# Kernel optimization log

Hardware: AMD Instinct MI355X
Metric: run time of the kernel (lower is better)

The kernel has to match this reference:

```python
import jax, jax.numpy as jnp
import numpy as np

B, T, D_MODEL, WINDOW = 2, 2048, 512, 32


def setup_inputs() -> dict:
    key = jax.random.key(0)
    ks = jax.random.split(key, 5)
    s = 1.0 / np.sqrt(D_MODEL)
    x = jax.random.normal(ks[0], (B, T, D_MODEL), jnp.float32)
    # torch.nn.Linear convention: weight [out_features, in_features], y = x @ W.T + b
    w_qkv = jax.random.uniform(ks[1], (3 * D_MODEL, D_MODEL), jnp.float32, -s, s)
    b_qkv = jax.random.uniform(ks[2], (3 * D_MODEL,), jnp.float32, -s, s)
    w_proj = jax.random.uniform(ks[3], (D_MODEL, D_MODEL), jnp.float32, -s, s)
    b_proj = jax.random.uniform(ks[4], (D_MODEL,), jnp.float32, -s, s)
    return {"x": x, "w_qkv": w_qkv, "b_qkv": b_qkv, "w_proj": w_proj, "b_proj": b_proj}


def reference(x, w_qkv, b_qkv, w_proj, b_proj):
    Bb, Tt, C = x.shape
    qkv = x @ w_qkv.T + b_qkv                      # [B,T,3C]
    q, k, v = jnp.split(qkv, 3, axis=-1)           # each [B,T,C]
    W = 2 * WINDOW - 1                             # non-causal window span [t-w+1, t+w-1]
    offs = jnp.arange(W) - (WINDOW - 1)            # [W]
    idx = jnp.arange(Tt)[:, None] + offs[None, :]  # [T,W] absolute key positions
    valid = (idx >= 0) & (idx < Tt)                # mask out-of-range window slots
    idx_c = jnp.clip(idx, 0, Tt - 1)
    k_win = k[:, idx_c]                            # [B,T,W,C]
    v_win = v[:, idx_c]                            # [B,T,W,C]
    scale = jnp.asarray(C, x.dtype) ** 0.5
    scores = jnp.einsum('btc,btwc->btw', q, k_win) / scale
    scores = jnp.where(valid[None], scores, -jnp.inf)
    p = jax.nn.softmax(scores, axis=-1)            # [B,T,W]
    out = jnp.einsum('btw,btwc->btc', p, v_win)    # [B,T,C]
    return out @ w_proj.T + b_proj
```

## Files before the change

### kernel.cpp

```cpp
#include <hip/hip_runtime.h>
#include <math.h>

#define BB 2
#define TT 2048
#define CC 512
#define WIN 32
#define WSZ 63
#define MM (BB * TT)

typedef __attribute__((ext_vector_type(8))) short short8;
typedef __attribute__((ext_vector_type(4))) float floatx4;

__device__ inline unsigned short bf16_rn(float f) {
  unsigned u = __builtin_bit_cast(unsigned, f);
  u += 0x7fff + ((u >> 16) & 1);
  return (unsigned short)(u >> 16);
}
__device__ inline unsigned pack_bf16x2(float lo, float hi) {
  return (unsigned)bf16_rn(lo) | ((unsigned)bf16_rn(hi) << 16);
}

#define NX  (MM * CC)
#define NWQ (3 * CC * CC)
#define NWP (CC * CC)

__global__ __launch_bounds__(256) void convert_bf16(
    const float* __restrict__ x, const float* __restrict__ wq,
    const float* __restrict__ wp, ushort* __restrict__ xb,
    ushort* __restrict__ wqb, ushort* __restrict__ wpb) {
  const size_t e = ((size_t)blockIdx.x * 256 + threadIdx.x) * 8;
  const float* src;
  ushort* dst;
  size_t off;
  if (e < NX) { src = x; dst = xb; off = e; }
  else if (e < NX + NWQ) { src = wq; dst = wqb; off = e - NX; }
  else { src = wp; dst = wpb; off = e - NX - NWQ; }
  float4 v0 = ((const float4*)(src + off))[0];
  float4 v1 = ((const float4*)(src + off))[1];
  uint4 o;
  o.x = pack_bf16x2(v0.x, v0.y);
  o.y = pack_bf16x2(v0.z, v0.w);
  o.z = pack_bf16x2(v1.x, v1.y);
  o.w = pack_bf16x2(v1.z, v1.w);
  *(uint4*)(dst + off) = o;
}

#define PSTR 264
#define VSTR 136

template <int BM, typename OT>
__global__ __launch_bounds__(256) void gemm_panel(
    const ushort* __restrict__ A, const ushort* __restrict__ B,
    const float* __restrict__ bias, OT* __restrict__ C,
    ushort* __restrict__ VT, int M, int N) {
  constexpr int MIW = BM / 64;
  __shared__ __align__(16) ushort Bs[64 * PSTR];

  const int tid = threadIdx.x;
  const int lane = tid & 63;
  const int wave = tid >> 6;
  const int m0 = blockIdx.y * BM;
  const int n0 = blockIdx.x * 64;
  const int wm = wave * (BM / 4);
  const int mlane = lane & 15, quad = lane >> 4;

  floatx4 acc[MIW][4];
#pragma unroll
  for (int i = 0; i < MIW; ++i)
#pragma unroll
    for (int j = 0; j < 4; ++j) acc[i][j] = (floatx4){0.f, 0.f, 0.f, 0.f};

  for (int h = 0; h < 2; ++h) {
    if (h) __syncthreads();
#pragma unroll
    for (int i = 0; i < 8; ++i) {
      const int idx = tid + 256 * i;
      const int r = idx >> 5, kc = (idx & 31) * 8;
      *(uint4*)(&Bs[r * PSTR + kc]) =
          *(const uint4*)(B + (size_t)(n0 + r) * CC + h * 256 + kc);
    }
    __syncthreads();
#pragma unroll
    for (int ks = 0; ks < 8; ++ks) {
      short8 bfr[4];
#pragma unroll
      for (int ni = 0; ni < 4; ++ni)
        bfr[ni] = *(const short8*)(&Bs[(ni * 16 + mlane) * PSTR + ks * 32 + quad * 8]);
#pragma unroll
      for (int mi = 0; mi < MIW; ++mi) {
        short8 af = *(const short8*)(
            A + (size_t)(m0 + wm + mi * 16 + mlane) * CC + h * 256 + ks * 32 + quad * 8);
#pragma unroll
        for (int ni = 0; ni < 4; ++ni)
          acc[mi][ni] = __builtin_amdgcn_mfma_f32_16x16x32_bf16(af, bfr[ni], acc[mi][ni], 0, 0, 0);
      }
    }
  }

  const bool vpath = (VT != nullptr) && (n0 >= 1024);
  if (!vpath) {
#pragma unroll
    for (int ni = 0; ni < 4; ++ni) {
      const int n = n0 + ni * 16 + mlane;
      const float bn = bias[n];
#pragma unroll
      for (int mi = 0; mi < MIW; ++mi) {
        const int mbase = m0 + wm + mi * 16 + quad * 4;
#pragma unroll
        for (int r = 0; r < 4; ++r) {
          float val = acc[mi][ni][r] + bn;
          if constexpr (sizeof(OT) == 2)
            ((ushort*)C)[(size_t)(mbase + r) * N + n] = bf16_rn(val);
          else
            ((float*)C)[(size_t)(mbase + r) * N + n] = val;
        }
      }
    }
  } else if constexpr (BM == 128) {
    ushort* Vt = Bs;
    __syncthreads();
#pragma unroll
    for (int ni = 0; ni < 4; ++ni) {
      const int n_l = ni * 16 + mlane;
      const float bn = bias[n0 + n_l];
#pragma unroll
      for (int mi = 0; mi < MIW; ++mi) {
        const int m_l = wm + mi * 16 + quad * 4;
        ushort4 pk;
        pk.x = bf16_rn(acc[mi][ni][0] + bn);
        pk.y = bf16_rn(acc[mi][ni][1] + bn);
        pk.z = bf16_rn(acc[mi][ni][2] + bn);
        pk.w = bf16_rn(acc[mi][ni][3] + bn);
        *(ushort4*)(&Vt[n_l * VSTR + m_l]) = pk;
      }
    }
    __syncthreads();
#pragma unroll
    for (int i = 0; i < 4; ++i) {
      const int idx = tid + 256 * i;
      const int n_l = idx >> 4, mo = (idx & 15) * 8;
      *(uint4*)(VT + (size_t)(n0 - 1024 + n_l) * M + m0 + mo) =
          *(const uint4*)(&Vt[n_l * VSTR + mo]);
    }
  }
}

#define ATILE 8
#define SLD 84
#define PLD 104

__global__ __launch_bounds__(256) void attn_mfma(
    const ushort* __restrict__ qkv, const ushort* __restrict__ vT,
    ushort* __restrict__ out) {
  __shared__ __align__(16) float s_s[16 * SLD];
  __shared__ __align__(16) ushort p_s[16 * PLD];

  const int tid = threadIdx.x;
  const int wave = tid >> 6, lane = tid & 63;
  const int mlane = lane & 15, quad = lane >> 4;
  const int bt0 = blockIdx.x * ATILE;
  const int b = bt0 / TT, t0 = bt0 % TT;
  const ushort* qbase = qkv + (size_t)b * TT * (3 * CC);

  const ushort* qrow  = qbase + (ptrdiff_t)(t0 + mlane) * (3 * CC);
  const ushort* krow0 = qbase + (ptrdiff_t)(t0 - 32 + wave * 16 + mlane) * (3 * CC) + CC;
  const ushort* krow1 = qbase + (ptrdiff_t)(t0 - 32 + 64 + mlane) * (3 * CC) + CC;
  floatx4 sacc0 = (floatx4){0.f, 0.f, 0.f, 0.f};
  floatx4 sacc1 = (floatx4){0.f, 0.f, 0.f, 0.f};
#pragma unroll
  for (int ks = 0; ks < 16; ++ks) {
    short8 a  = *(const short8*)(qrow + ks * 32 + quad * 8);
    short8 b0 = *(const short8*)(krow0 + ks * 32 + quad * 8);
    sacc0 = __builtin_amdgcn_mfma_f32_16x16x32_bf16(a, b0, sacc0, 0, 0, 0);
    if (wave == 0) {
      short8 b1 = *(const short8*)(krow1 + ks * 32 + quad * 8);
      sacc1 = __builtin_amdgcn_mfma_f32_16x16x32_bf16(a, b1, sacc1, 0, 0, 0);
    }
  }

#pragma unroll
  for (int r = 0; r < 4; ++r)
    s_s[(quad * 4 + r) * SLD + wave * 16 + mlane] = sacc0[r];
  if (wave == 0) {
#pragma unroll
    for (int r = 0; r < 4; ++r)
      s_s[(quad * 4 + r) * SLD + 64 + mlane] = sacc1[r];
  }
  __syncthreads();

  {
    const int row = tid >> 4, li = tid & 15;
    const float inv_scale = 0.044194173824159216f;
    float e[5];
    float mx = -INFINITY;
#pragma unroll
    for (int i = 0; i < 5; ++i) {
      const int r = li + 16 * i;
      const int j = r - 1 - row;
      const int src = t0 - 32 + r;
      const bool valid = (j >= 0) && (j < WSZ) && (src >= 0) && (src < TT);
      e[i] = valid ? s_s[row * SLD + r] * inv_scale : -INFINITY;
      mx = fmaxf(mx, e[i]);
    }
    mx = fmaxf(mx, __shfl_xor(mx, 1)); mx = fmaxf(mx, __shfl_xor(mx, 2));
    mx = fmaxf(mx, __shfl_xor(mx, 4)); mx = fmaxf(mx, __shfl_xor(mx, 8));
    float sum = 0.f;
#pragma unroll
    for (int i = 0; i < 5; ++i) {
      e[i] = (e[i] == -INFINITY) ? 0.f : __expf(e[i] - mx);
      sum += e[i];
    }
    sum += __shfl_xor(sum, 1); sum += __shfl_xor(sum, 2);
    sum += __shfl_xor(sum, 4); sum += __shfl_xor(sum, 8);
    const float rs = 1.f / sum;
#pragma unroll
    for (int i = 0; i < 5; ++i)
      p_s[row * PLD + li + 16 * i] = bf16_rn(e[i] * rs);
    if (li < 8) {
      p_s[row * PLD + 80 + li] = 0;
      p_s[row * PLD + 88 + li] = 0;
      p_s[row * PLD + 96 + li] = 0;
    }
  }
  __syncthreads();

  const ptrdiff_t mcol0 = (ptrdiff_t)b * TT + t0 - 32;
#pragma unroll 2
  for (int nt8 = 0; nt8 < 8; ++nt8) {
    const int nt = wave * 8 + nt8;
    const ushort* vrow = vT + (ptrdiff_t)(nt * 16 + mlane) * MM + mcol0;
    floatx4 o = (floatx4){0.f, 0.f, 0.f, 0.f};
#pragma unroll
    for (int ks = 0; ks < 3; ++ks) {
      short8 a  = *(const short8*)(&p_s[mlane * PLD + ks * 32 + quad * 8]);
      short8 bv = *(const short8*)(vrow + ks * 32 + quad * 8);
      o = __builtin_amdgcn_mfma_f32_16x16x32_bf16(a, bv, o, 0, 0, 0);
    }
    if (quad < 2) {
#pragma unroll
      for (int r = 0; r < 4; ++r)
        out[(size_t)(bt0 + quad * 4 + r) * CC + nt * 16 + mlane] = bf16_rn(o[r]);
    }
  }
}

extern "C" void kernel_launch(void* const* d_in, const int* in_sizes, int n_in,
                              void* d_out, int out_size, void* d_ws, size_t ws_size,
                              hipStream_t stream) {
  const float* x      = (const float*)d_in[0];
  const float* w_qkv  = (const float*)d_in[1];
  const float* b_qkv  = (const float*)d_in[2];
  const float* w_proj = (const float*)d_in[3];
  const float* b_proj = (const float*)d_in[4];
  float* outp = (float*)d_out;

  ushort* base  = (ushort*)d_ws;
  ushort* qkv   = base + 131072;
  ushort* attn  = qkv + (size_t)MM * 3 * CC;
  ushort* xb    = attn + (size_t)MM * CC;
  ushort* wqb   = xb + (size_t)NX;
  ushort* wpb   = wqb + (size_t)NWQ;
  ushort* vTg   = wpb + (size_t)NWP;
  ushort* vT    = vTg + 64;

  convert_bf16<<<(NX + NWQ + NWP) / (256 * 8), 256, 0, stream>>>(x, w_qkv, w_proj, xb, wqb, wpb);
  {
    dim3 grid((3 * CC) / 64, MM / 128);
    gemm_panel<128, ushort><<<grid, 256, 0, stream>>>(xb, wqb, b_qkv, qkv, vT, MM, 3 * CC);
  }
  attn_mfma<<<MM / ATILE, 256, 0, stream>>>(qkv, vT, attn);
  {
    dim3 grid(CC / 64, MM / 64);
    gemm_panel<64, float><<<grid, 256, 0, stream>>>(attn, wpb, b_proj, outp, nullptr, MM, CC);
  }
}
```

Before: 114.9 us.

## Fuse weight bf16 conversion into GEMM loads and shrink QKV buffer stride

Drops the separate weight conversion pass: each GEMM block now reads fp32 weights and converts them to bf16 while staging into shared memory, leaving only x to convert up front. The QKV GEMM switches to 64-row tiles, and the q/k buffer drops the unused V columns (stride 1024), since V already goes to a transposed buffer. The attention kernel splits the score accumulation into two interleaved MFMA chains and hoists the P fragment loads out of the V loop. In exchange, each block re-converts weights redundantly, and smaller tiles reload weight panels more often.

```diff
diff --git a/kernel.cpp b/kernel.cpp
--- a/kernel.cpp
+++ b/kernel.cpp
@@ -7,6 +7,7 @@
 #define WIN 32
 #define WSZ 63
 #define MM (BB * TT)
+#define QKLD 1024
 
 typedef __attribute__((ext_vector_type(8))) short short8;
 typedef __attribute__((ext_vector_type(4))) float floatx4;
@@ -20,55 +21,43 @@
   return (unsigned)bf16_rn(lo) | ((unsigned)bf16_rn(hi) << 16);
 }
 
-#define NX  (MM * CC)
-#define NWQ (3 * CC * CC)
-#define NWP (CC * CC)
-
-__global__ __launch_bounds__(256) void convert_bf16(
-    const float* __restrict__ x, const float* __restrict__ wq,
-    const float* __restrict__ wp, ushort* __restrict__ xb,
-    ushort* __restrict__ wqb, ushort* __restrict__ wpb) {
+#define NX (MM * CC)
+
+__global__ __launch_bounds__(256) void convert_x(
+    const float* __restrict__ x, ushort* __restrict__ xb) {
   const size_t e = ((size_t)blockIdx.x * 256 + threadIdx.x) * 8;
-  const float* src;
-  ushort* dst;
-  size_t off;
-  if (e < NX) { src = x; dst = xb; off = e; }
-  else if (e < NX + NWQ) { src = wq; dst = wqb; off = e - NX; }
-  else { src = wp; dst = wpb; off = e - NX - NWQ; }
-  float4 v0 = ((const float4*)(src + off))[0];
-  float4 v1 = ((const float4*)(src + off))[1];
+  float4 v0 = ((const float4*)(x + e))[0];
+  float4 v1 = ((const float4*)(x + e))[1];
   uint4 o;
   o.x = pack_bf16x2(v0.x, v0.y);
   o.y = pack_bf16x2(v0.z, v0.w);
   o.z = pack_bf16x2(v1.x, v1.y);
   o.w = pack_bf16x2(v1.z, v1.w);
-  *(uint4*)(dst + off) = o;
+  *(uint4*)(xb + e) = o;
 }
 
 #define PSTR 264
-#define VSTR 136
-
-template <int BM, typename OT>
+#define VSTR 80
+
+template <typename OT>
 __global__ __launch_bounds__(256) void gemm_panel(
-    const ushort* __restrict__ A, const ushort* __restrict__ B,
-    const float* __restrict__ bias, OT* __restrict__ C,
-    ushort* __restrict__ VT, int M, int N) {
-  constexpr int MIW = BM / 64;
+    const ushort* __restrict__ A, const float* __restrict__ Bf,
+    const float* __restrict__ bias, OT* __restrict__ C, int ldC,
+    ushort* __restrict__ VT, int M) {
   __shared__ __align__(16) ushort Bs[64 * PSTR];
 
   const int tid = threadIdx.x;
   const int lane = tid & 63;
   const int wave = tid >> 6;
-  const int m0 = blockIdx.y * BM;
+  const int m0 = blockIdx.y * 64;
   const int n0 = blockIdx.x * 64;
-  const int wm = wave * (BM / 4);
   const int mlane = lane & 15, quad = lane >> 4;
 
-  floatx4 acc[MIW][4];
-#pragma unroll
-  for (int i = 0; i < MIW; ++i)
-#pragma unroll
-    for (int j = 0; j < 4; ++j) acc[i][j] = (floatx4){0.f, 0.f, 0.f, 0.f};
+  floatx4 acc[4];
+#pragma unroll
+  for (int j = 0; j < 4; ++j) acc[j] = (floatx4){0.f, 0.f, 0.f, 0.f};
+
+  const ushort* arow = A + (size_t)(m0 + wave * 16 + mlane) * CC;
 
   for (int h = 0; h < 2; ++h) {
     if (h) __syncthreads();
@@ -76,69 +65,64 @@
     for (int i = 0; i < 8; ++i) {
       const int idx = tid + 256 * i;
       const int r = idx >> 5, kc = (idx & 31) * 8;
-      *(uint4*)(&Bs[r * PSTR + kc]) =
-          *(const uint4*)(B + (size_t)(n0 + r) * CC + h * 256 + kc);
+      const float* src = Bf + (size_t)(n0 + r) * CC + h * 256 + kc;
+      float4 v0 = ((const float4*)src)[0];
+      float4 v1 = ((const float4*)src)[1];
+      uint4 o;
+      o.x = pack_bf16x2(v0.x, v0.y);
+      o.y = pack_bf16x2(v0.z, v0.w);
+      o.z = pack_bf16x2(v1.x, v1.y);
+      o.w = pack_bf16x2(v1.z, v1.w);
+      *(uint4*)(&Bs[r * PSTR + kc]) = o;
     }
     __syncthreads();
 #pragma unroll
     for (int ks = 0; ks < 8; ++ks) {
-      short8 bfr[4];
-#pragma unroll
-      for (int ni = 0; ni < 4; ++ni)
-        bfr[ni] = *(const short8*)(&Bs[(ni * 16 + mlane) * PSTR + ks * 32 + quad * 8]);
-#pragma unroll
-      for (int mi = 0; mi < MIW; ++mi) {
-        short8 af = *(const short8*)(
-            A + (size_t)(m0 + wm + mi * 16 + mlane) * CC + h * 256 + ks * 32 + quad * 8);
-#pragma unroll
-        for (int ni = 0; ni < 4; ++ni)
-          acc[mi][ni] = __builtin_amdgcn_mfma_f32_16x16x32_bf16(af, bfr[ni], acc[mi][ni], 0, 0, 0);
+      short8 af = *(const short8*)(arow + h * 256 + ks * 32 + quad * 8);
+#pragma unroll
+      for (int ni = 0; ni < 4; ++ni) {
+        short8 bfr = *(const short8*)(&Bs[(ni * 16 + mlane) * PSTR + ks * 32 + quad * 8]);
+        acc[ni] = __builtin_amdgcn_mfma_f32_16x16x32_bf16(af, bfr, acc[ni], 0, 0, 0);
       }
     }
   }
 
   const bool vpath = (VT != nullptr) && (n0 >= 1024);
   if (!vpath) {
+    const int mbase = m0 + wave * 16 + quad * 4;
 #pragma unroll
     for (int ni = 0; ni < 4; ++ni) {
       const int n = n0 + ni * 16 + mlane;
       const float bn = bias[n];
 #pragma unroll
-      for (int mi = 0; mi < MIW; ++mi) {
-        const int mbase = m0 + wm + mi * 16 + quad * 4;
-#pragma unroll
-        for (int r = 0; r < 4; ++r) {
-          float val = acc[mi][ni][r] + bn;
-          if constexpr (sizeof(OT) == 2)
-            ((ushort*)C)[(size_t)(mbase + r) * N + n] = bf16_rn(val);
-          else
-            ((float*)C)[(size_t)(mbase + r) * N + n] = val;
-        }
+      for (int r = 0; r < 4; ++r) {
+        float val = acc[ni][r] + bn;
+        if constexpr (sizeof(OT) == 2)
+          ((ushort*)C)[(size_t)(mbase + r) * ldC + n] = bf16_rn(val);
+        else
+          ((float*)C)[(size_t)(mbase + r) * ldC + n] = val;
       }
     }
-  } else if constexpr (BM == 128) {
+  } else {
     ushort* Vt = Bs;
     __syncthreads();
+    const int m_l = wave * 16 + quad * 4;
 #pragma unroll
     for (int ni = 0; ni < 4; ++ni) {
       const int n_l = ni * 16 + mlane;
       const float bn = bias[n0 + n_l];
-#pragma unroll
-      for (int mi = 0; mi < MIW; ++mi) {
-        const int m_l = wm + mi * 16 + quad * 4;
-        ushort4 pk;
-        pk.x = bf16_rn(acc[mi][ni][0] + bn);
-        pk.y = bf16_rn(acc[mi][ni][1] + bn);
-        pk.z = bf16_rn(acc[mi][ni][2] + bn);
-        pk.w = bf16_rn(acc[mi][ni][3] + bn);
-        *(ushort4*)(&Vt[n_l * VSTR + m_l]) = pk;
-      }
+      ushort4 pk;
+      pk.x = bf16_rn(acc[ni][0] + bn);
+      pk.y = bf16_rn(acc[ni][1] + bn);
+      pk.z = bf16_rn(acc[ni][2] + bn);
+      pk.w = bf16_rn(acc[ni][3] + bn);
+      *(ushort4*)(&Vt[n_l * VSTR + m_l]) = pk;
     }
     __syncthreads();
 #pragma unroll
-    for (int i = 0; i < 4; ++i) {
+    for (int i = 0; i < 2; ++i) {
       const int idx = tid + 256 * i;
-      const int n_l = idx >> 4, mo = (idx & 15) * 8;
+      const int n_l = idx >> 3, mo = (idx & 7) * 8;
       *(uint4*)(VT + (size_t)(n0 - 1024 + n_l) * M + m0 + mo) =
           *(const uint4*)(&Vt[n_l * VSTR + mo]);
     }
@@ -160,31 +144,33 @@
   const int mlane = lane & 15, quad = lane >> 4;
   const int bt0 = blockIdx.x * ATILE;
   const int b = bt0 / TT, t0 = bt0 % TT;
-  const ushort* qbase = qkv + (size_t)b * TT * (3 * CC);
-
-  const ushort* qrow  = qbase + (ptrdiff_t)(t0 + mlane) * (3 * CC);
-  const ushort* krow0 = qbase + (ptrdiff_t)(t0 - 32 + wave * 16 + mlane) * (3 * CC) + CC;
-  const ushort* krow1 = qbase + (ptrdiff_t)(t0 - 32 + 64 + mlane) * (3 * CC) + CC;
-  floatx4 sacc0 = (floatx4){0.f, 0.f, 0.f, 0.f};
-  floatx4 sacc1 = (floatx4){0.f, 0.f, 0.f, 0.f};
+  const ushort* qbase = qkv + (size_t)b * TT * QKLD;
+
+  const ushort* qrow  = qbase + (ptrdiff_t)(t0 + mlane) * QKLD;
+  const ushort* krow0 = qbase + (ptrdiff_t)(t0 - 32 + wave * 16 + mlane) * QKLD + CC;
+  const ushort* krow1 = qbase + (ptrdiff_t)(t0 - 32 + 64 + mlane) * QKLD + CC;
+  floatx4 s0a = (floatx4){0.f, 0.f, 0.f, 0.f}, s0b = s0a;
+  floatx4 s1a = s0a, s1b = s0a;
 #pragma unroll
   for (int ks = 0; ks < 16; ++ks) {
     short8 a  = *(const short8*)(qrow + ks * 32 + quad * 8);
     short8 b0 = *(const short8*)(krow0 + ks * 32 + quad * 8);
-    sacc0 = __builtin_amdgcn_mfma_f32_16x16x32_bf16(a, b0, sacc0, 0, 0, 0);
+    if (ks & 1) s0b = __builtin_amdgcn_mfma_f32_16x16x32_bf16(a, b0, s0b, 0, 0, 0);
+    else        s0a = __builtin_amdgcn_mfma_f32_16x16x32_bf16(a, b0, s0a, 0, 0, 0);
     if (wave == 0) {
       short8 b1 = *(const short8*)(krow1 + ks * 32 + quad * 8);
-      sacc1 = __builtin_amdgcn_mfma_f32_16x16x32_bf16(a, b1, sacc1, 0, 0, 0);
+      if (ks & 1) s1b = __builtin_amdgcn_mfma_f32_16x16x32_bf16(a, b1, s1b, 0, 0, 0);
+      else        s1a = __builtin_amdgcn_mfma_f32_16x16x32_bf16(a, b1, s1a, 0, 0, 0);
     }
   }
 
 #pragma unroll
   for (int r = 0; r < 4; ++r)
-    s_s[(quad * 4 + r) * SLD + wave * 16 + mlane] = sacc0[r];
+    s_s[(quad * 4 + r) * SLD + wave * 16 + mlane] = s0a[r] + s0b[r];
   if (wave == 0) {
 #pragma unroll
     for (int r = 0; r < 4; ++r)
-      s_s[(quad * 4 + r) * SLD + 64 + mlane] = sacc1[r];
+      s_s[(quad * 4 + r) * SLD + 64 + mlane] = s1a[r] + s1b[r];
   }
   __syncthreads();
 
@@ -225,6 +211,10 @@
   __syncthreads();
 
   const ptrdiff_t mcol0 = (ptrdiff_t)b * TT + t0 - 32;
+  short8 pa[3];
+#pragma unroll
+  for (int ks = 0; ks < 3; ++ks)
+    pa[ks] = *(const short8*)(&p_s[mlane * PLD + ks * 32 + quad * 8]);
 #pragma unroll 2
   for (int nt8 = 0; nt8 < 8; ++nt8) {
     const int nt = wave * 8 + nt8;
@@ -232,9 +222,8 @@
     floatx4 o = (floatx4){0.f, 0.f, 0.f, 0.f};
 #pragma unroll
     for (int ks = 0; ks < 3; ++ks) {
-      short8 a  = *(const short8*)(&p_s[mlane * PLD + ks * 32 + quad * 8]);
       short8 bv = *(const short8*)(vrow + ks * 32 + quad * 8);
-      o = __builtin_amdgcn_mfma_f32_16x16x32_bf16(a, bv, o, 0, 0, 0);
+      o = __builtin_amdgcn_mfma_f32_16x16x32_bf16(pa[ks], bv, o, 0, 0, 0);
     }
     if (quad < 2) {
 #pragma unroll
@@ -256,21 +245,19 @@
 
   ushort* base  = (ushort*)d_ws;
   ushort* qkv   = base + 131072;
-  ushort* attn  = qkv + (size_t)MM * 3 * CC;
+  ushort* attn  = qkv + (size_t)MM * QKLD;
   ushort* xb    = attn + (size_t)MM * CC;
-  ushort* wqb   = xb + (size_t)NX;
-  ushort* wpb   = wqb + (size_t)NWQ;
-  ushort* vTg   = wpb + (size_t)NWP;
+  ushort* vTg   = xb + (size_t)NX;
   ushort* vT    = vTg + 64;
 
-  convert_bf16<<<(NX + NWQ + NWP) / (256 * 8), 256, 0, stream>>>(x, w_qkv, w_proj, xb, wqb, wpb);
+  convert_x<<<NX / (256 * 8), 256, 0, stream>>>(x, xb);
   {
-    dim3 grid((3 * CC) / 64, MM / 128);
-    gemm_panel<128, ushort><<<grid, 256, 0, stream>>>(xb, wqb, b_qkv, qkv, vT, MM, 3 * CC);
+    dim3 grid((3 * CC) / 64, MM / 64);
+    gemm_panel<ushort><<<grid, 256, 0, stream>>>(xb, w_qkv, b_qkv, qkv, QKLD, vT, MM);
   }
   attn_mfma<<<MM / ATILE, 256, 0, stream>>>(qkv, vT, attn);
   {
     dim3 grid(CC / 64, MM / 64);
-    gemm_panel<64, float><<<grid, 256, 0, stream>>>(attn, wpb, b_proj, outp, nullptr, MM, CC);
-  }
-}
+    gemm_panel<float><<<grid, 256, 0, stream>>>(attn, w_proj, b_proj, outp, CC, nullptr, MM);
+  }
+}
```

New measurement: 132.4 us. 1.15x slower.

## Fuse output projection into attention kernel and shrink QKV buffer stride

Applied to the files above, without the earlier changes.

The separate projection GEMM launch is removed. Each attention block now stages its 8-row attention output in shared memory and multiplies it by w_proj, reading the weight rows straight from global memory. The QKV buffer stride drops to 1024 because V is already stored transposed elsewhere, and the QK score accumulation is split into two chains to raise MFMA ILP. The trade-off is that each 8-row block reloads the full 512x512 projection weight, and half of each 16-row MFMA tile is wasted, so the extra weight traffic and compute may outweigh the saved launch and intermediate round trip.

```diff
diff --git a/kernel.cpp b/kernel.cpp
--- a/kernel.cpp
+++ b/kernel.cpp
@@ -7,6 +7,7 @@
 #define WIN 32
 #define WSZ 63
 #define MM (BB * TT)
+#define QKLD 1024
 
 typedef __attribute__((ext_vector_type(8))) short short8;
 typedef __attribute__((ext_vector_type(4))) float floatx4;
@@ -48,25 +49,23 @@
 #define PSTR 264
 #define VSTR 136
 
-template <int BM, typename OT>
-__global__ __launch_bounds__(256) void gemm_panel(
+__global__ __launch_bounds__(256) void gemm_qkv(
     const ushort* __restrict__ A, const ushort* __restrict__ B,
-    const float* __restrict__ bias, OT* __restrict__ C,
-    ushort* __restrict__ VT, int M, int N) {
-  constexpr int MIW = BM / 64;
+    const float* __restrict__ bias, ushort* __restrict__ C,
+    ushort* __restrict__ VT) {
   __shared__ __align__(16) ushort Bs[64 * PSTR];
 
   const int tid = threadIdx.x;
   const int lane = tid & 63;
   const int wave = tid >> 6;
-  const int m0 = blockIdx.y * BM;
+  const int m0 = blockIdx.y * 128;
   const int n0 = blockIdx.x * 64;
-  const int wm = wave * (BM / 4);
+  const int wm = wave * 32;
   const int mlane = lane & 15, quad = lane >> 4;
 
-  floatx4 acc[MIW][4];
-#pragma unroll
-  for (int i = 0; i < MIW; ++i)
+  floatx4 acc[2][4];
+#pragma unroll
+  for (int i = 0; i < 2; ++i)
 #pragma unroll
     for (int j = 0; j < 4; ++j) acc[i][j] = (floatx4){0.f, 0.f, 0.f, 0.f};
 
@@ -87,7 +86,7 @@
       for (int ni = 0; ni < 4; ++ni)
         bfr[ni] = *(const short8*)(&Bs[(ni * 16 + mlane) * PSTR + ks * 32 + quad * 8]);
 #pragma unroll
-      for (int mi = 0; mi < MIW; ++mi) {
+      for (int mi = 0; mi < 2; ++mi) {
         short8 af = *(const short8*)(
             A + (size_t)(m0 + wm + mi * 16 + mlane) * CC + h * 256 + ks * 32 + quad * 8);
 #pragma unroll
@@ -97,26 +96,20 @@
     }
   }
 
-  const bool vpath = (VT != nullptr) && (n0 >= 1024);
-  if (!vpath) {
+  if (n0 < 1024) {
 #pragma unroll
     for (int ni = 0; ni < 4; ++ni) {
       const int n = n0 + ni * 16 + mlane;
       const float bn = bias[n];
 #pragma unroll
-      for (int mi = 0; mi < MIW; ++mi) {
+      for (int mi = 0; mi < 2; ++mi) {
         const int mbase = m0 + wm + mi * 16 + quad * 4;
 #pragma unroll
-        for (int r = 0; r < 4; ++r) {
-          float val = acc[mi][ni][r] + bn;
-          if constexpr (sizeof(OT) == 2)
-            ((ushort*)C)[(size_t)(mbase + r) * N + n] = bf16_rn(val);
-          else
-            ((float*)C)[(size_t)(mbase + r) * N + n] = val;
-        }
-      }
-    }
-  } else if constexpr (BM == 128) {
+        for (int r = 0; r < 4; ++r)
+          C[(size_t)(mbase + r) * QKLD + n] = bf16_rn(acc[mi][ni][r] + bn);
+      }
+    }
+  } else {
     ushort* Vt = Bs;
     __syncthreads();
 #pragma unroll
@@ -124,7 +117,7 @@
       const int n_l = ni * 16 + mlane;
       const float bn = bias[n0 + n_l];
 #pragma unroll
-      for (int mi = 0; mi < MIW; ++mi) {
+      for (int mi = 0; mi < 2; ++mi) {
         const int m_l = wm + mi * 16 + quad * 4;
         ushort4 pk;
         pk.x = bf16_rn(acc[mi][ni][0] + bn);
@@ -139,7 +132,7 @@
     for (int i = 0; i < 4; ++i) {
       const int idx = tid + 256 * i;
       const int n_l = idx >> 4, mo = (idx & 15) * 8;
-      *(uint4*)(VT + (size_t)(n0 - 1024 + n_l) * M + m0 + mo) =
+      *(uint4*)(VT + (size_t)(n0 - 1024 + n_l) * MM + m0 + mo) =
           *(const uint4*)(&Vt[n_l * VSTR + mo]);
     }
   }
@@ -148,43 +141,48 @@
 #define ATILE 8
 #define SLD 84
 #define PLD 104
-
-__global__ __launch_bounds__(256) void attn_mfma(
+#define ATS 520
+
+__global__ __launch_bounds__(256) void attn_proj(
     const ushort* __restrict__ qkv, const ushort* __restrict__ vT,
-    ushort* __restrict__ out) {
+    const ushort* __restrict__ wpb, const float* __restrict__ bproj,
+    float* __restrict__ out) {
   __shared__ __align__(16) float s_s[16 * SLD];
   __shared__ __align__(16) ushort p_s[16 * PLD];
+  __shared__ __align__(16) ushort at_s[16 * ATS];
 
   const int tid = threadIdx.x;
   const int wave = tid >> 6, lane = tid & 63;
   const int mlane = lane & 15, quad = lane >> 4;
   const int bt0 = blockIdx.x * ATILE;
   const int b = bt0 / TT, t0 = bt0 % TT;
-  const ushort* qbase = qkv + (size_t)b * TT * (3 * CC);
-
-  const ushort* qrow  = qbase + (ptrdiff_t)(t0 + mlane) * (3 * CC);
-  const ushort* krow0 = qbase + (ptrdiff_t)(t0 - 32 + wave * 16 + mlane) * (3 * CC) + CC;
-  const ushort* krow1 = qbase + (ptrdiff_t)(t0 - 32 + 64 + mlane) * (3 * CC) + CC;
-  floatx4 sacc0 = (floatx4){0.f, 0.f, 0.f, 0.f};
-  floatx4 sacc1 = (floatx4){0.f, 0.f, 0.f, 0.f};
+  const ushort* qbase = qkv + (size_t)b * TT * QKLD;
+
+  const ushort* qrow  = qbase + (ptrdiff_t)(t0 + mlane) * QKLD;
+  const ushort* krow0 = qbase + (ptrdiff_t)(t0 - 32 + wave * 16 + mlane) * QKLD + CC;
+  const ushort* krow1 = qbase + (ptrdiff_t)(t0 - 32 + 64 + mlane) * QKLD + CC;
+  floatx4 s0a = (floatx4){0.f, 0.f, 0.f, 0.f}, s0b = s0a;
+  floatx4 s1a = s0a, s1b = s0a;
 #pragma unroll
   for (int ks = 0; ks < 16; ++ks) {
     short8 a  = *(const short8*)(qrow + ks * 32 + quad * 8);
     short8 b0 = *(const short8*)(krow0 + ks * 32 + quad * 8);
-    sacc0 = __builtin_amdgcn_mfma_f32_16x16x32_bf16(a, b0, sacc0, 0, 0, 0);
+    if (ks & 1) s0b = __builtin_amdgcn_mfma_f32_16x16x32_bf16(a, b0, s0b, 0, 0, 0);
+    else        s0a = __builtin_amdgcn_mfma_f32_16x16x32_bf16(a, b0, s0a, 0, 0, 0);
     if (wave == 0) {
       short8 b1 = *(const short8*)(krow1 + ks * 32 + quad * 8);
-      sacc1 = __builtin_amdgcn_mfma_f32_16x16x32_bf16(a, b1, sacc1, 0, 0, 0);
+      if (ks & 1) s1b = __builtin_amdgcn_mfma_f32_16x16x32_bf16(a, b1, s1b, 0, 0, 0);
+      else        s1a = __builtin_amdgcn_mfma_f32_16x16x32_bf16(a, b1, s1a, 0, 0, 0);
     }
   }
 
 #pragma unroll
   for (int r = 0; r < 4; ++r)
-    s_s[(quad * 4 + r) * SLD + wave * 16 + mlane] = sacc0[r];
+    s_s[(quad * 4 + r) * SLD + wave * 16 + mlane] = s0a[r] + s0b[r];
   if (wave == 0) {
 #pragma unroll
     for (int r = 0; r < 4; ++r)
-      s_s[(quad * 4 + r) * SLD + 64 + mlane] = sacc1[r];
+      s_s[(quad * 4 + r) * SLD + 64 + mlane] = s1a[r] + s1b[r];
   }
   __syncthreads();
 
@@ -225,21 +223,49 @@
   __syncthreads();
 
   const ptrdiff_t mcol0 = (ptrdiff_t)b * TT + t0 - 32;
-#pragma unroll 2
-  for (int nt8 = 0; nt8 < 8; ++nt8) {
-    const int nt = wave * 8 + nt8;
-    const ushort* vrow = vT + (ptrdiff_t)(nt * 16 + mlane) * MM + mcol0;
-    floatx4 o = (floatx4){0.f, 0.f, 0.f, 0.f};
-#pragma unroll
-    for (int ks = 0; ks < 3; ++ks) {
-      short8 a  = *(const short8*)(&p_s[mlane * PLD + ks * 32 + quad * 8]);
-      short8 bv = *(const short8*)(vrow + ks * 32 + quad * 8);
-      o = __builtin_amdgcn_mfma_f32_16x16x32_bf16(a, bv, o, 0, 0, 0);
-    }
-    if (quad < 2) {
+  {
+    short8 pa[3];
+#pragma unroll
+    for (int ks = 0; ks < 3; ++ks)
+      pa[ks] = *(const short8*)(&p_s[mlane * PLD + ks * 32 + quad * 8]);
+#pragma unroll
+    for (int nt8 = 0; nt8 < 8; ++nt8) {
+      const int nt = wave * 8 + nt8;
+      const ushort* vrow = vT + (ptrdiff_t)(nt * 16 + mlane) * MM + mcol0;
+      floatx4 o = (floatx4){0.f, 0.f, 0.f, 0.f};
+#pragma unroll
+      for (int ks = 0; ks < 3; ++ks) {
+        short8 bv = *(const short8*)(vrow + ks * 32 + quad * 8);
+        o = __builtin_amdgcn_mfma_f32_16x16x32_bf16(pa[ks], bv, o, 0, 0, 0);
+      }
 #pragma unroll
       for (int r = 0; r < 4; ++r)
-        out[(size_t)(bt0 + quad * 4 + r) * CC + nt * 16 + mlane] = bf16_rn(o[r]);
+        at_s[(quad * 4 + r) * ATS + nt * 16 + mlane] = bf16_rn(o[r]);
+    }
+  }
+  __syncthreads();
+
+  {
+    short8 af[16];
+#pragma unroll
+    for (int ks = 0; ks < 16; ++ks)
+      af[ks] = *(const short8*)(&at_s[mlane * ATS + ks * 32 + quad * 8]);
+#pragma unroll
+    for (int i = 0; i < 8; ++i) {
+      const int n = (wave * 8 + i) * 16 + mlane;
+      const ushort* wrow = wpb + (size_t)n * CC;
+      floatx4 o = (floatx4){0.f, 0.f, 0.f, 0.f};
+#pragma unroll
+      for (int ks = 0; ks < 16; ++ks) {
+        short8 bfr = *(const short8*)(wrow + ks * 32 + quad * 8);
+        o = __builtin_amdgcn_mfma_f32_16x16x32_bf16(af[ks], bfr, o, 0, 0, 0);
+      }
+      if (quad < 2) {
+        const float bn = bproj[n];
+#pragma unroll
+        for (int r = 0; r < 4; ++r)
+          out[(size_t)(bt0 + quad * 4 + r) * CC + n] = o[r] + bn;
+      }
     }
   }
 }
@@ -256,8 +282,7 @@
 
   ushort* base  = (ushort*)d_ws;
   ushort* qkv   = base + 131072;
-  ushort* attn  = qkv + (size_t)MM * 3 * CC;
-  ushort* xb    = attn + (size_t)MM * CC;
+  ushort* xb    = qkv + (size_t)MM * QKLD;
   ushort* wqb   = xb + (size_t)NX;
   ushort* wpb   = wqb + (size_t)NWQ;
   ushort* vTg   = wpb + (size_t)NWP;
@@ -266,11 +291,7 @@
   convert_bf16<<<(NX + NWQ + NWP) / (256 * 8), 256, 0, stream>>>(x, w_qkv, w_proj, xb, wqb, wpb);
   {
     dim3 grid((3 * CC) / 64, MM / 128);
-    gemm_panel<128, ushort><<<grid, 256, 0, stream>>>(xb, wqb, b_qkv, qkv, vT, MM, 3 * CC);
-  }
-  attn_mfma<<<MM / ATILE, 256, 0, stream>>>(qkv, vT, attn);
-  {
-    dim3 grid(CC / 64, MM / 64);
-    gemm_panel<64, float><<<grid, 256, 0, stream>>>(attn, wpb, b_proj, outp, nullptr, MM, CC);
-  }
-}
+    gemm_qkv<<<grid, 256, 0, stream>>>(xb, wqb, b_qkv, qkv, vT);
+  }
+  attn_proj<<<MM / ATILE, 256, 0, stream>>>(qkv, vT, wpb, b_proj, outp);
+}
```

Measured after the change: 132.9 us. 15.7% more time.
